# Optimization experiments

Hardware: AMD Instinct MI355X
Metric: run time of the kernel (lower is better)

## Reference

```python
import jax, jax.numpy as jnp
import numpy as np

B, S, D = 16, 2048, 512
MAX_DIST = 32.0
NEG_SAMPLES = 4
MARGIN = 20


def _make_indices(seq_len, margin, neg_samples, seed=0):
    """Replicates the Python-loop index sampling of SignCL.forward.

    Anchors are i in [1, seq_len-3]. Positives are always {i-1, i+1}
    (random.sample with k=2 from 2 elements selects both). Negatives are
    neg_samples indices drawn without replacement from [2, seq_len-3] with
    idx < i-margin or idx > i+margin.
    """
    rng = np.random.RandomState(seed)
    anchors = np.arange(1, seq_len - 2)
    pos_idx = np.stack([anchors - 1, anchors + 1], axis=1)  # (A, 2)
    neg_idx = np.empty((anchors.shape[0], neg_samples), dtype=np.int64)
    for j, i in enumerate(anchors):
        lo = np.arange(2, max(2, i - margin))
        hi = np.arange(max(2, i + margin + 1), seq_len - 2)
        valid = np.concatenate([lo, hi])
        neg_idx[j] = rng.choice(valid, size=neg_samples, replace=False)
    return pos_idx, neg_idx


def setup_inputs() -> dict:
    key = jax.random.key(0)
    inputs_embeds = jax.random.normal(key, (B, S, D), dtype=jnp.float32)
    pos_np, neg_np = _make_indices(S, MARGIN, NEG_SAMPLES, seed=0)
    return {
        "inputs_embeds": inputs_embeds,
        "pos_idx": jnp.asarray(pos_np, dtype=jnp.int64 if jax.config.jax_enable_x64 else jnp.int32),
        "neg_idx": jnp.asarray(neg_np, dtype=jnp.int64 if jax.config.jax_enable_x64 else jnp.int32),
        "margin": MARGIN,
    }


def reference(inputs_embeds, pos_idx, neg_idx, margin):
    # margin was already consumed when building neg_idx (data-independent sampling).
    b, s, d = inputs_embeds.shape
    anchors = inputs_embeds[:, 1:s - 2, :]                    # (B, A, D)
    positives = inputs_embeds[:, pos_idx, :]                  # (B, A, 2, D)
    negatives = inputs_embeds[:, neg_idx, :]                  # (B, A, 4, D)
    pos_dist = jnp.sum(jnp.abs(anchors[:, :, None, :] - positives), axis=-1)  # (B, A, 2)
    neg_dist = jnp.sum(jnp.abs(anchors[:, :, None, :] - negatives), axis=-1)  # (B, A, 4)
    pos_loss = jax.nn.softplus(pos_dist - MAX_DIST).mean(axis=(0, 2))  # (A,) per-anchor mean over batch & samples
    neg_loss = jax.nn.softplus(MAX_DIST - neg_dist).mean(axis=(0, 2))
    total_loss = jnp.sum(pos_loss + neg_loss)
    return total_loss / (b * (s - 4))
```

## Files before the change

kernel.cpp:

```cpp
#include <hip/hip_runtime.h>
#include <math.h>

constexpr int Bc = 16;
constexpr int Sc = 2048;
constexpr int Dc = 512;
constexpr int NA = Sc - 3;
constexpr float MAXD = 32.0f;

constexpr int ITEMS_PER_XCD = 2 * NA;
constexpr int BLK_PER_XCD = (ITEMS_PER_XCD + 3) / 4;
constexpr int NBLK = 8 * BLK_PER_XCD;

__device__ __forceinline__ float softplus_fast(float x) {
    return fmaxf(x, 0.0f) + __logf(1.0f + __expf(-fabsf(x)));
}

template <int CTRL, int RMASK>
__device__ __forceinline__ float dpp_add(float x) {
    int y = __builtin_amdgcn_update_dpp(0, __float_as_int(x), CTRL, RMASK, 0xF, true);
    return x + __int_as_float(y);
}

__device__ __forceinline__ void wave_reduce6(float p[6]) {
#pragma unroll
    for (int t = 0; t < 6; ++t) p[t] = dpp_add<0xB1, 0xF>(p[t]);
#pragma unroll
    for (int t = 0; t < 6; ++t) p[t] = dpp_add<0x4E, 0xF>(p[t]);
#pragma unroll
    for (int t = 0; t < 6; ++t) p[t] = dpp_add<0x141, 0xF>(p[t]);
#pragma unroll
    for (int t = 0; t < 6; ++t) p[t] = dpp_add<0x140, 0xF>(p[t]);
#pragma unroll
    for (int t = 0; t < 6; ++t) p[t] = dpp_add<0x142, 0xA>(p[t]);
#pragma unroll
    for (int t = 0; t < 6; ++t) p[t] = dpp_add<0x143, 0xC>(p[t]);
}

__global__ __launch_bounds__(256) void signcl_kernel(
    const float* __restrict__ x,
    const int* __restrict__ pos_idx,
    const int* __restrict__ neg_idx,
    float* __restrict__ partials)
{
    const int lane = threadIdx.x & 63;
    const int wib  = threadIdx.x >> 6;
    const int xcd  = blockIdx.x & 7;
    const int sub  = blockIdx.x >> 3;
    const int item = sub * 4 + wib;
    const bool valid = item < ITEMS_PER_XCD;

    float acc = 0.0f;
    if (valid) {
        const int bb = (item >= NA) ? 1 : 0;
        const int a  = item - bb * NA;
        const int b  = xcd + 8 * bb;

        const float* base = x + (size_t)b * Sc * Dc;
        const float4* av =
            reinterpret_cast<const float4*>(base + (size_t)(a + 1) * Dc);
        const float4 a0 = av[2 * lane];
        const float4 a1 = av[2 * lane + 1];

        int idx[6];
        idx[0] = __builtin_amdgcn_readfirstlane(pos_idx[2 * a]);
        idx[1] = __builtin_amdgcn_readfirstlane(pos_idx[2 * a + 1]);
#pragma unroll
        for (int t = 0; t < 4; ++t)
            idx[2 + t] = __builtin_amdgcn_readfirstlane(neg_idx[4 * a + t]);

        float part[6];
#pragma unroll
        for (int t = 0; t < 6; ++t) {
            const float4* tv =
                reinterpret_cast<const float4*>(base + (size_t)idx[t] * Dc);
            const float4 t0 = tv[2 * lane];
            const float4 t1 = tv[2 * lane + 1];
            part[t] = fabsf(a0.x - t0.x) + fabsf(a0.y - t0.y)
                    + fabsf(a0.z - t0.z) + fabsf(a0.w - t0.w)
                    + fabsf(a1.x - t1.x) + fabsf(a1.y - t1.y)
                    + fabsf(a1.z - t1.z) + fabsf(a1.w - t1.w);
        }

        wave_reduce6(part);

        if (lane == 63) {
            const float wpos =
                1.0f / ((float)Bc * 2.0f * (float)Bc * (float)(Sc - 4));
            const float wneg =
                1.0f / ((float)Bc * 4.0f * (float)Bc * (float)(Sc - 4));
            acc = wpos * (softplus_fast(part[0] - MAXD) +
                          softplus_fast(part[1] - MAXD))
                + wneg * (softplus_fast(MAXD - part[2]) +
                          softplus_fast(MAXD - part[3]) +
                          softplus_fast(MAXD - part[4]) +
                          softplus_fast(MAXD - part[5]));
        }
    }

    __shared__ float wsum[4];
    if (lane == 63) wsum[wib] = acc;
    __syncthreads();
    if (threadIdx.x == 0)
        partials[blockIdx.x] = wsum[0] + wsum[1] + wsum[2] + wsum[3];
}

__global__ __launch_bounds__(1024) void signcl_finalize(
    const float* __restrict__ partials, float* __restrict__ out)
{
    const int tid = threadIdx.x;
    float acc = 0.0f;
#pragma unroll
    for (int k = 0; k < 8; ++k) {
        int i = tid + k * 1024;
        if (i < NBLK) acc += partials[i];
    }

    float p[6] = {acc, 0, 0, 0, 0, 0};
    wave_reduce6(p);
    __shared__ float smem[16];
    if ((tid & 63) == 63) smem[tid >> 6] = p[0];
    __syncthreads();
    if (tid == 0) {
        float s = 0.0f;
#pragma unroll
        for (int i = 0; i < 16; ++i) s += smem[i];
        out[0] = s;
    }
}

extern "C" void kernel_launch(void* const* d_in, const int* in_sizes, int n_in,
                              void* d_out, int out_size, void* d_ws, size_t ws_size,
                              hipStream_t stream) {
    const float* x   = (const float*)d_in[0];
    const int*   pos = (const int*)d_in[1];
    const int*   neg = (const int*)d_in[2];
    float* out = (float*)d_out;
    float* partials = (float*)d_ws;

    signcl_kernel<<<NBLK, 256, 0, stream>>>(x, pos, neg, partials);
    signcl_finalize<<<1, 1024, 0, stream>>>(partials, out);
}
```

Baseline: 110.4 us.

## Process two adjacent anchors per wave and share positive-neighbor rows

Each wave now handles a pair of consecutive anchors. It loads the four contiguous rows a0..a0+3 once and derives both anchors' positive distances from them, so the shared middle distance is computed once and weighted twice. Positives are taken as the fixed a-1/a+1 neighbors instead of being gathered through pos_idx, and the negative indices are read as int4 vectors. The finalize kernel is simplified to a single float4 load per thread. This cuts the number of row gathers and waves per anchor, at the cost of more registers per wave and a hardcoded assumption about the positive-index structure.

```diff
diff --git a/kernel.cpp b/kernel.cpp
--- a/kernel.cpp
+++ b/kernel.cpp
@@ -7,9 +7,10 @@
 constexpr int NA = Sc - 3;
 constexpr float MAXD = 32.0f;
 
-constexpr int ITEMS_PER_XCD = 2 * NA;
-constexpr int BLK_PER_XCD = (ITEMS_PER_XCD + 3) / 4;
-constexpr int NBLK = 8 * BLK_PER_XCD;
+constexpr int PAIRS_PER_BATCH = (NA + 1) / 2;
+constexpr int PAIRS_PER_XCD   = 2 * PAIRS_PER_BATCH;
+constexpr int BLK_PER_XCD     = (PAIRS_PER_XCD + 3) / 4;
+constexpr int NBLK            = 8 * BLK_PER_XCD;
 
 __device__ __forceinline__ float softplus_fast(float x) {
     return fmaxf(x, 0.0f) + __logf(1.0f + __expf(-fabsf(x)));
@@ -21,24 +22,32 @@
     return x + __int_as_float(y);
 }
 
-__device__ __forceinline__ void wave_reduce6(float p[6]) {
+template <int N>
+__device__ __forceinline__ void wave_reduceN(float p[N]) {
 #pragma unroll
-    for (int t = 0; t < 6; ++t) p[t] = dpp_add<0xB1, 0xF>(p[t]);
+    for (int t = 0; t < N; ++t) p[t] = dpp_add<0xB1, 0xF>(p[t]);
 #pragma unroll
-    for (int t = 0; t < 6; ++t) p[t] = dpp_add<0x4E, 0xF>(p[t]);
+    for (int t = 0; t < N; ++t) p[t] = dpp_add<0x4E, 0xF>(p[t]);
 #pragma unroll
-    for (int t = 0; t < 6; ++t) p[t] = dpp_add<0x141, 0xF>(p[t]);
+    for (int t = 0; t < N; ++t) p[t] = dpp_add<0x141, 0xF>(p[t]);
 #pragma unroll
-    for (int t = 0; t < 6; ++t) p[t] = dpp_add<0x140, 0xF>(p[t]);
+    for (int t = 0; t < N; ++t) p[t] = dpp_add<0x140, 0xF>(p[t]);
 #pragma unroll
-    for (int t = 0; t < 6; ++t) p[t] = dpp_add<0x142, 0xA>(p[t]);
+    for (int t = 0; t < N; ++t) p[t] = dpp_add<0x142, 0xA>(p[t]);
 #pragma unroll
-    for (int t = 0; t < 6; ++t) p[t] = dpp_add<0x143, 0xC>(p[t]);
+    for (int t = 0; t < N; ++t) p[t] = dpp_add<0x143, 0xC>(p[t]);
+}
+
+__device__ __forceinline__ float l1_8(const float4& a0, const float4& a1,
+                                      const float4& b0, const float4& b1) {
+    return fabsf(a0.x - b0.x) + fabsf(a0.y - b0.y)
+         + fabsf(a0.z - b0.z) + fabsf(a0.w - b0.w)
+         + fabsf(a1.x - b1.x) + fabsf(a1.y - b1.y)
+         + fabsf(a1.z - b1.z) + fabsf(a1.w - b1.w);
 }
 
 __global__ __launch_bounds__(256) void signcl_kernel(
     const float* __restrict__ x,
-    const int* __restrict__ pos_idx,
     const int* __restrict__ neg_idx,
     float* __restrict__ partials)
 {
@@ -46,54 +55,79 @@
     const int wib  = threadIdx.x >> 6;
     const int xcd  = blockIdx.x & 7;
     const int sub  = blockIdx.x >> 3;
-    const int item = sub * 4 + wib;
-    const bool valid = item < ITEMS_PER_XCD;
+    const int pairId = sub * 4 + wib;
+    const bool valid = pairId < PAIRS_PER_XCD;
 
     float acc = 0.0f;
     if (valid) {
-        const int bb = (item >= NA) ? 1 : 0;
-        const int a  = item - bb * NA;
-        const int b  = xcd + 8 * bb;
+        const int bb = (pairId >= PAIRS_PER_BATCH) ? 1 : 0;
+        const int pp = pairId - bb * PAIRS_PER_BATCH;
+        const int a0 = 2 * pp;
+        const bool pair = (a0 + 1) < NA;
+        const float pairf = pair ? 1.0f : 0.0f;
+        const int b = xcd + 8 * bb;
 
         const float* base = x + (size_t)b * Sc * Dc;
-        const float4* av =
-            reinterpret_cast<const float4*>(base + (size_t)(a + 1) * Dc);
-        const float4 a0 = av[2 * lane];
-        const float4 a1 = av[2 * lane + 1];
 
-        int idx[6];
-        idx[0] = __builtin_amdgcn_readfirstlane(pos_idx[2 * a]);
-        idx[1] = __builtin_amdgcn_readfirstlane(pos_idx[2 * a + 1]);
+        const float4* rv[4];
+#pragma unroll
+        for (int r = 0; r < 4; ++r)
+            rv[r] = reinterpret_cast<const float4*>(base + (size_t)(a0 + r) * Dc);
+        float4 row0[4], row1[4];
+#pragma unroll
+        for (int r = 0; r < 4; ++r) {
+            row0[r] = rv[r][2 * lane];
+            row1[r] = rv[r][2 * lane + 1];
+        }
+
+        const int a1c = pair ? (a0 + 1) : a0;
+        const int4 n0v = *reinterpret_cast<const int4*>(neg_idx + 4 * a0);
+        const int4 n1v = *reinterpret_cast<const int4*>(neg_idx + 4 * a1c);
+        int nidx[8];
+        nidx[0] = __builtin_amdgcn_readfirstlane(n0v.x);
+        nidx[1] = __builtin_amdgcn_readfirstlane(n0v.y);
+        nidx[2] = __builtin_amdgcn_readfirstlane(n0v.z);
+        nidx[3] = __builtin_amdgcn_readfirstlane(n0v.w);
+        nidx[4] = __builtin_amdgcn_readfirstlane(n1v.x);
+        nidx[5] = __builtin_amdgcn_readfirstlane(n1v.y);
+        nidx[6] = __builtin_amdgcn_readfirstlane(n1v.z);
+        nidx[7] = __builtin_amdgcn_readfirstlane(n1v.w);
+
+        float4 neg0[8], neg1[8];
+#pragma unroll
+        for (int t = 0; t < 8; ++t) {
+            const float4* tv =
+                reinterpret_cast<const float4*>(base + (size_t)nidx[t] * Dc);
+            neg0[t] = tv[2 * lane];
+            neg1[t] = tv[2 * lane + 1];
+        }
+
+        float d[11];
+        d[0] = l1_8(row0[1], row1[1], row0[0], row1[0]);
+        d[1] = l1_8(row0[1], row1[1], row0[2], row1[2]);
+        d[2] = l1_8(row0[2], row1[2], row0[3], row1[3]);
 #pragma unroll
         for (int t = 0; t < 4; ++t)
-            idx[2 + t] = __builtin_amdgcn_readfirstlane(neg_idx[4 * a + t]);
+            d[3 + t] = l1_8(row0[1], row1[1], neg0[t], neg1[t]);
+#pragma unroll
+        for (int t = 0; t < 4; ++t)
+            d[7 + t] = l1_8(row0[2], row1[2], neg0[4 + t], neg1[4 + t]);
 
-        float part[6];
-#pragma unroll
-        for (int t = 0; t < 6; ++t) {
-            const float4* tv =
-                reinterpret_cast<const float4*>(base + (size_t)idx[t] * Dc);
-            const float4 t0 = tv[2 * lane];
-            const float4 t1 = tv[2 * lane + 1];
-            part[t] = fabsf(a0.x - t0.x) + fabsf(a0.y - t0.y)
-                    + fabsf(a0.z - t0.z) + fabsf(a0.w - t0.w)
-                    + fabsf(a1.x - t1.x) + fabsf(a1.y - t1.y)
-                    + fabsf(a1.z - t1.z) + fabsf(a1.w - t1.w);
-        }
-
-        wave_reduce6(part);
+        wave_reduceN<11>(d);
 
         if (lane == 63) {
             const float wpos =
                 1.0f / ((float)Bc * 2.0f * (float)Bc * (float)(Sc - 4));
             const float wneg =
                 1.0f / ((float)Bc * 4.0f * (float)Bc * (float)(Sc - 4));
-            acc = wpos * (softplus_fast(part[0] - MAXD) +
-                          softplus_fast(part[1] - MAXD))
-                + wneg * (softplus_fast(MAXD - part[2]) +
-                          softplus_fast(MAXD - part[3]) +
-                          softplus_fast(MAXD - part[4]) +
-                          softplus_fast(MAXD - part[5]));
+            float pos = softplus_fast(d[0] - MAXD)
+                      + (1.0f + pairf) * softplus_fast(d[1] - MAXD)
+                      + pairf * softplus_fast(d[2] - MAXD);
+            float neg_a = softplus_fast(MAXD - d[3]) + softplus_fast(MAXD - d[4])
+                        + softplus_fast(MAXD - d[5]) + softplus_fast(MAXD - d[6]);
+            float neg_b = softplus_fast(MAXD - d[7]) + softplus_fast(MAXD - d[8])
+                        + softplus_fast(MAXD - d[9]) + softplus_fast(MAXD - d[10]);
+            acc = wpos * pos + wneg * (neg_a + pairf * neg_b);
         }
     }
 
@@ -108,15 +142,9 @@
     const float* __restrict__ partials, float* __restrict__ out)
 {
     const int tid = threadIdx.x;
-    float acc = 0.0f;
-#pragma unroll
-    for (int k = 0; k < 8; ++k) {
-        int i = tid + k * 1024;
-        if (i < NBLK) acc += partials[i];
-    }
-
-    float p[6] = {acc, 0, 0, 0, 0, 0};
-    wave_reduce6(p);
+    const float4 v = reinterpret_cast<const float4*>(partials)[tid];
+    float p[1] = {v.x + v.y + v.z + v.w};
+    wave_reduceN<1>(p);
     __shared__ float smem[16];
     if ((tid & 63) == 63) smem[tid >> 6] = p[0];
     __syncthreads();
@@ -132,11 +160,10 @@
                               void* d_out, int out_size, void* d_ws, size_t ws_size,
                               hipStream_t stream) {
     const float* x   = (const float*)d_in[0];
-    const int*   pos = (const int*)d_in[1];
     const int*   neg = (const int*)d_in[2];
     float* out = (float*)d_out;
     float* partials = (float*)d_ws;
 
-    signcl_kernel<<<NBLK, 256, 0, stream>>>(x, pos, neg, partials);
+    signcl_kernel<<<NBLK, 256, 0, stream>>>(x, neg, partials);
     signcl_finalize<<<1, 1024, 0, stream>>>(partials, out);
 }
```

Measured after the change: 110.6 us. No clear change (+0.2%).
